# Optimization experiments

Hardware: AMD Instinct MI355X
Metric: run time of the kernel (lower is better)

Reference implementation:

```python
import jax, jax.numpy as jnp
import numpy as np
from jax import lax

UNITS = 64
LAYERS = 4

def _lstm_layer(x, Wx, U, b):
    # x: [B,T,F]; Keras gate order i,f,c,o; activation=relu, recurrent_activation=sigmoid
    B = x.shape[0]
    xz = jnp.einsum('btf,fg->btg', x, Wx) + b  # precompute input projections [B,T,4U]
    def step(carry, xz_t):
        h, c = carry
        z = xz_t + h @ U
        i, f, g, o = jnp.split(z, 4, axis=-1)
        c = jax.nn.sigmoid(f) * c + jax.nn.sigmoid(i) * jax.nn.relu(g)
        h = jax.nn.sigmoid(o) * jax.nn.relu(c)
        return (h, c), h
    h0 = jnp.zeros((B, UNITS), dtype=x.dtype)
    c0 = jnp.zeros((B, UNITS), dtype=x.dtype)
    _, hs = lax.scan(step, (h0, c0), jnp.swapaxes(xz, 0, 1))
    return jnp.swapaxes(hs, 0, 1)  # [B,T,U]

def setup_inputs() -> dict:
    key = jax.random.key(0)
    ks = jax.random.split(key, 1 + 3 * LAYERS + 2)
    B, T, F = 1024, 512, 1
    d = {'x': jax.random.normal(ks[0], (B, T, F), dtype=jnp.float32)}
    fin = F
    for l in range(LAYERS):
        d[f'Wx{l}'] = jax.random.normal(ks[1 + 3 * l], (fin, 4 * UNITS), dtype=jnp.float32) * 0.05
        d[f'U{l}'] = jax.random.normal(ks[2 + 3 * l], (UNITS, 4 * UNITS), dtype=jnp.float32) * 0.05
        d[f'b{l}'] = jnp.zeros((4 * UNITS,), dtype=jnp.float32)
        fin = UNITS
    d['Wd'] = jax.random.normal(ks[-2], (UNITS, 1), dtype=jnp.float32) * 0.05
    d['bd'] = jnp.zeros((1,), dtype=jnp.float32)
    return d

def reference(x, Wx0, U0, b0, Wx1, U1, b1, Wx2, U2, b2, Wx3, U3, b3, Wd, bd):
    # Dropout is identity at inference.
    h = x
    for Wx, U, b in ((Wx0, U0, b0), (Wx1, U1, b1), (Wx2, U2, b2), (Wx3, U3, b3)):
        h = _lstm_layer(h, Wx, U, b)
    h_last = h[:, -1, :]  # return_sequences=False on last LSTM
    return h_last @ Wd + bd  # [B,1]
```

## Files before the change

kernel.cpp:

```cpp
#include <hip/hip_runtime.h>
#include <stdint.h>

#define TT 512

typedef __fp16   f16x8  __attribute__((ext_vector_type(8)));
typedef float    f32x4  __attribute__((ext_vector_type(4)));
typedef __fp16   fp16x2 __attribute__((ext_vector_type(2)));
typedef uint32_t u32x2  __attribute__((ext_vector_type(2)));

__device__ __forceinline__ f32x4 mfma16(f16x8 a, f16x8 b, f32x4 c) {
    return __builtin_amdgcn_mfma_f32_16x16x32_f16(a, b, c, 0, 0, 0);
}
__device__ __forceinline__ uint32_t pkf16(float a, float b) {
    fp16x2 h = __builtin_amdgcn_cvt_pkrtz(a, b);
    return __builtin_bit_cast(uint32_t, h);
}

#define REP8(M) M(0)M(1)M(2)M(3)M(4)M(5)M(6)M(7)

#define GA(SRC, T, F) (f16x8){ \
  (__fp16)(SRC)[(32*(F)+8*quad+0)*256 + 16*(T)+l15], \
  (__fp16)(SRC)[(32*(F)+8*quad+1)*256 + 16*(T)+l15], \
  (__fp16)(SRC)[(32*(F)+8*quad+2)*256 + 16*(T)+l15], \
  (__fp16)(SRC)[(32*(F)+8*quad+3)*256 + 16*(T)+l15], \
  (__fp16)(SRC)[(32*(F)+8*quad+4)*256 + 16*(T)+l15], \
  (__fp16)(SRC)[(32*(F)+8*quad+5)*256 + 16*(T)+l15], \
  (__fp16)(SRC)[(32*(F)+8*quad+6)*256 + 16*(T)+l15], \
  (__fp16)(SRC)[(32*(F)+8*quad+7)*256 + 16*(T)+l15] }

#define DECLT(j) f16x8 uA##j##_0, uA##j##_1, wA##j##_0, wA##j##_1; f32x4 bias##j;
#define LOADT(j) { \
  const int Tg_ = ((j)>>1)*4 + 2*h + ((j)&1); \
  uA##j##_0 = GA(Uw, Tg_, 0); uA##j##_1 = GA(Uw, Tg_, 1); \
  bias##j = (f32x4){ bw_[16*Tg_ + 4*quad + 0], bw_[16*Tg_ + 4*quad + 1], \
                     bw_[16*Tg_ + 4*quad + 2], bw_[16*Tg_ + 4*quad + 3] }; \
  if (l > 0) { wA##j##_0 = GA(Wsrc, Tg_, 0); wA##j##_1 = GA(Wsrc, Tg_, 1); } \
  else { wA##j##_0 = __builtin_bit_cast(f16x8, (f32x4){ \
           Wx0[16*Tg_+4*quad+0], Wx0[16*Tg_+4*quad+1], \
           Wx0[16*Tg_+4*quad+2], Wx0[16*Tg_+4*quad+3] }); \
         wA##j##_1 = wA##j##_0; } }

#define MW0(j) acc##j = mfma16(wA##j##_0, xBp0, bias##j);
#define MW1(j) acc##j = mfma16(wA##j##_1, xBp1, acc##j);
#define MX(j)  acc##j = bias##j + __builtin_bit_cast(f32x4, wA##j##_0) * xvp4;
#define MU0(j) acc##j = mfma16(uA##j##_0, hB0, acc##j);
#define MU1(j) acc##j = mfma16(uA##j##_1, hB1, acc##j);

#define MFMA_SEG(t_) { \
  const __fp16* hp_ = hb_l + (((t_)-1)&3)*1152 + l15*72 + 8*quad; \
  f16x8 hB0 = *(const f16x8*)hp_; \
  f16x8 hB1 = *(const f16x8*)(hp_ + 32); \
  if (l > 0) { REP8(MW0) REP8(MW1) } \
  else       { f32x4 xvp4 = {xvp, xvp, xvp, xvp}; REP8(MX) } \
  REP8(MU0) \
  REP8(MU1) }

#define GATES(qp, Ai, Af, Ag, Ao, CST, SAVEK, HK) { \
  f32x4 ei_, ef_, eo_; \
  _Pragma("unroll") for (int r_ = 0; r_ < 4; ++r_) { \
    ei_[r_] = __builtin_amdgcn_exp2f(-1.4426950408889634f * Ai[r_]); \
    ef_[r_] = __builtin_amdgcn_exp2f(-1.4426950408889634f * Af[r_]); \
    eo_[r_] = __builtin_amdgcn_exp2f(-1.4426950408889634f * Ao[r_]); \
  } \
  f32x4 si_, sf_, so_; \
  _Pragma("unroll") for (int r_ = 0; r_ < 4; ++r_) { \
    si_[r_] = __builtin_amdgcn_rcpf(1.0f + ei_[r_]); \
    sf_[r_] = __builtin_amdgcn_rcpf(1.0f + ef_[r_]); \
    so_[r_] = __builtin_amdgcn_rcpf(1.0f + eo_[r_]); \
  } \
  const f32x4 z4_ = {0.f, 0.f, 0.f, 0.f}; \
  f32x4 rg_ = __builtin_elementwise_max(Ag, z4_); \
  f32x4 cv_ = sf_ * CST + si_ * rg_; \
  CST = cv_; \
  f32x4 hv_ = so_ * __builtin_elementwise_max(cv_, z4_); \
  u32x2 pv_ = { pkf16(hv_[0], hv_[1]), pkf16(hv_[2], hv_[3]) }; \
  *(u32x2*)(hw_ + 16*(qp)) = pv_; \
  if (SAVEK) HK = hv_; }

#define GATE_SEG(tg_, SV_) { \
  __fp16* hw_ = hb_l + ((tg_)&3)*1152 + l15*72 + 32*h + 4*quad; \
  GATES(0, acc0, acc2, acc4, acc6, cst0, SV_, hK0) \
  GATES(1, acc1, acc3, acc5, acc7, cst1, SV_, hK1) }

__global__ __launch_bounds__(512)
__attribute__((amdgpu_waves_per_eu(2, 2)))
void lstm_phase(
    const float* __restrict__ x,
    const float* __restrict__ Wx0, const float* __restrict__ U0, const float* __restrict__ b0,
    const float* __restrict__ Wx1, const float* __restrict__ U1, const float* __restrict__ b1,
    const float* __restrict__ Wx2, const float* __restrict__ U2, const float* __restrict__ b2,
    const float* __restrict__ Wx3, const float* __restrict__ U3, const float* __restrict__ b3,
    const float* __restrict__ Wd,  const float* __restrict__ bd,
    float* __restrict__ out)
{
    extern __shared__ uint32_t smem[];
    __fp16* hb16 = (__fp16*)smem;
    float*  xs   = (float*)(smem + 9216);
    float*  red  = (float*)(smem + 17920);

    const int tid  = threadIdx.x;
    const int lane = tid & 63;
    const int l15  = lane & 15;
    const int quad = lane >> 4;
    const int wv   = tid >> 6;
    const int l    = wv >> 1;
    const int h    = wv & 1;
    const int b0i  = blockIdx.x * 16;
    const bool phA = (l < 2);

    for (int i = tid; i < 9216; i += 512) smem[i] = 0;
    for (int i = tid; i < 16 * TT; i += 512) {
        int row = i >> 9, t_ = i & (TT - 1);
        xs[t_ * 17 + row] = x[(b0i + row) * TT + t_];
    }

    const float* Uw   = (l == 0) ? U0 : (l == 1) ? U1 : (l == 2) ? U2 : U3;
    const float* bw_  = (l == 0) ? b0 : (l == 1) ? b1 : (l == 2) ? b2 : b3;
    const float* Wsrc = (l == 1) ? Wx1 : (l == 2) ? Wx2 : (l == 3) ? Wx3 : U0;

    REP8(DECLT)
    REP8(LOADT)

    f32x4 acc0, acc1, acc2, acc3, acc4, acc5, acc6, acc7;
    f32x4 cst0 = {0,0,0,0}, cst1 = {0,0,0,0};
    f32x4 hK0  = {0,0,0,0}, hK1  = {0,0,0,0};

    __fp16* hb_l  = hb16 + l * 4608;
    const __fp16* hb_in = hb16 + (l > 0 ? (l - 1) * 4608 : 0);

    f16x8 xBp0 = {}, xBp1 = {};
    float xvp = 0.f;

    __syncthreads();

    if (l == 0) xvp = xs[l15];

    for (int s = 0; s < TT + 8; ++s) {
        if (phA) {
            const int t = s - 2 * l;
            if (t >= 0 && t < TT) MFMA_SEG(t)
        } else {
            const int tm = s - 2 * l;
            if (tm >= 0 && tm < TT) {
                const __fp16* xp_ = hb_in + (tm & 3) * 1152 + l15 * 72 + 8 * quad;
                xBp0 = *(const f16x8*)xp_;
                xBp1 = *(const f16x8*)(xp_ + 32);
            }
            const int tg = s - 1 - 2 * l;
            if (tg >= 0 && tg < TT) {
                const bool sv_ = (l == 3) && (tg == TT - 1);
                GATE_SEG(tg, sv_)
            }
        }
        __syncthreads();
        if (phA) {
            const int tn = s + 1 - 2 * l;
            if (tn >= 0 && tn < TT) {
                if (l > 0) {
                    const __fp16* xp_ = hb_in + (tn & 3) * 1152 + l15 * 72 + 8 * quad;
                    xBp0 = *(const f16x8*)xp_;
                    xBp1 = *(const f16x8*)(xp_ + 32);
                } else {
                    xvp = xs[tn * 17 + l15];
                }
            }
            const int t = s - 2 * l;
            if (t >= 0 && t < TT) GATE_SEG(t, false)
        } else {
            const int t = s - 2 * l;
            if (t >= 0 && t < TT) MFMA_SEG(t)
        }
        __syncthreads();
    }

    if (l == 3) {
        float p = 0.f;
        #pragma unroll
        for (int r = 0; r < 4; ++r) {
            p += hK0[r] * Wd[32 * h + 4 * quad + r];
            p += hK1[r] * Wd[32 * h + 16 + 4 * quad + r];
        }
        p += __shfl_down(p, 32, 64);
        p += __shfl_down(p, 16, 64);
        if (lane < 16) red[h * 16 + lane] = p;
    }
    __syncthreads();
    if (wv == 6 && lane < 16) out[b0i + lane] = red[lane] + red[16 + lane] + bd[0];
}

extern "C" void kernel_launch(void* const* d_in, const int* in_sizes, int n_in,
                              void* d_out, int out_size, void* d_ws, size_t ws_size,
                              hipStream_t stream) {
    const float* x   = (const float*)d_in[0];
    const float* Wx0 = (const float*)d_in[1];
    const float* U0  = (const float*)d_in[2];
    const float* b0  = (const float*)d_in[3];
    const float* Wx1 = (const float*)d_in[4];
    const float* U1  = (const float*)d_in[5];
    const float* b1  = (const float*)d_in[6];
    const float* Wx2 = (const float*)d_in[7];
    const float* U2  = (const float*)d_in[8];
    const float* b2  = (const float*)d_in[9];
    const float* Wx3 = (const float*)d_in[10];
    const float* U3  = (const float*)d_in[11];
    const float* b3  = (const float*)d_in[12];
    const float* Wd  = (const float*)d_in[13];
    const float* bd  = (const float*)d_in[14];
    float* out = (float*)d_out;

    static const int kLds = 17952 * 4;
    (void)hipFuncSetAttribute((const void*)lstm_phase,
                              hipFuncAttributeMaxDynamicSharedMemorySize, kLds);
    hipLaunchKernelGGL(lstm_phase, dim3(64), dim3(512), kLds, stream,
                       x, Wx0, U0, b0, Wx1, U1, b1, Wx2, U2, b2, Wx3, U3, b3,
                       Wd, bd, out);
}
```

Measured before the change: 691.9 us.

## Split each LSTM layer across four waves and move biases to LDS

Doubles the block to 1024 threads so each layer is handled by four waves instead of two. Each wave now owns one 16-column tile per gate rather than two, which halves the per-wave MFMA chain and gate math on the serial recurrence. Biases move from registers into shared memory and are reloaded every step, which frees registers for the higher waves-per-EU target. In exchange, more waves contend at every __syncthreads, and the final reduction now sums four partials.

```diff
diff --git a/kernel.cpp b/kernel.cpp
--- a/kernel.cpp
+++ b/kernel.cpp
@@ -16,7 +16,7 @@
     return __builtin_bit_cast(uint32_t, h);
 }
 
-#define REP8(M) M(0)M(1)M(2)M(3)M(4)M(5)M(6)M(7)
+#define REP4(M) M(0)M(1)M(2)M(3)
 
 #define GA(SRC, T, F) (f16x8){ \
   (__fp16)(SRC)[(32*(F)+8*quad+0)*256 + 16*(T)+l15], \
@@ -28,12 +28,10 @@
   (__fp16)(SRC)[(32*(F)+8*quad+6)*256 + 16*(T)+l15], \
   (__fp16)(SRC)[(32*(F)+8*quad+7)*256 + 16*(T)+l15] }
 
-#define DECLT(j) f16x8 uA##j##_0, uA##j##_1, wA##j##_0, wA##j##_1; f32x4 bias##j;
+#define DECLT(j) f16x8 uA##j##_0, uA##j##_1, wA##j##_0, wA##j##_1;
 #define LOADT(j) { \
-  const int Tg_ = ((j)>>1)*4 + 2*h + ((j)&1); \
+  const int Tg_ = 4*(j) + h2; \
   uA##j##_0 = GA(Uw, Tg_, 0); uA##j##_1 = GA(Uw, Tg_, 1); \
-  bias##j = (f32x4){ bw_[16*Tg_ + 4*quad + 0], bw_[16*Tg_ + 4*quad + 1], \
-                     bw_[16*Tg_ + 4*quad + 2], bw_[16*Tg_ + 4*quad + 3] }; \
   if (l > 0) { wA##j##_0 = GA(Wsrc, Tg_, 0); wA##j##_1 = GA(Wsrc, Tg_, 1); } \
   else { wA##j##_0 = __builtin_bit_cast(f16x8, (f32x4){ \
            Wx0[16*Tg_+4*quad+0], Wx0[16*Tg_+4*quad+1], \
@@ -47,15 +45,20 @@
 #define MU1(j) acc##j = mfma16(uA##j##_1, hB1, acc##j);
 
 #define MFMA_SEG(t_) { \
+  const float* bp_ = bs + l*256 + 16*h2 + 4*quad; \
+  f32x4 bias0 = *(const f32x4*)(bp_ +   0); \
+  f32x4 bias1 = *(const f32x4*)(bp_ +  64); \
+  f32x4 bias2 = *(const f32x4*)(bp_ + 128); \
+  f32x4 bias3 = *(const f32x4*)(bp_ + 192); \
   const __fp16* hp_ = hb_l + (((t_)-1)&3)*1152 + l15*72 + 8*quad; \
   f16x8 hB0 = *(const f16x8*)hp_; \
   f16x8 hB1 = *(const f16x8*)(hp_ + 32); \
-  if (l > 0) { REP8(MW0) REP8(MW1) } \
-  else       { f32x4 xvp4 = {xvp, xvp, xvp, xvp}; REP8(MX) } \
-  REP8(MU0) \
-  REP8(MU1) }
-
-#define GATES(qp, Ai, Af, Ag, Ao, CST, SAVEK, HK) { \
+  if (l > 0) { REP4(MW0) REP4(MW1) } \
+  else       { f32x4 xvp4 = {xvp, xvp, xvp, xvp}; REP4(MX) } \
+  REP4(MU0) \
+  REP4(MU1) }
+
+#define GATES(Ai, Af, Ag, Ao, CST, SAVEK, HK) { \
   f32x4 ei_, ef_, eo_; \
   _Pragma("unroll") for (int r_ = 0; r_ < 4; ++r_) { \
     ei_[r_] = __builtin_amdgcn_exp2f(-1.4426950408889634f * Ai[r_]); \
@@ -74,16 +77,15 @@
   CST = cv_; \
   f32x4 hv_ = so_ * __builtin_elementwise_max(cv_, z4_); \
   u32x2 pv_ = { pkf16(hv_[0], hv_[1]), pkf16(hv_[2], hv_[3]) }; \
-  *(u32x2*)(hw_ + 16*(qp)) = pv_; \
+  *(u32x2*)(hw_) = pv_; \
   if (SAVEK) HK = hv_; }
 
 #define GATE_SEG(tg_, SV_) { \
-  __fp16* hw_ = hb_l + ((tg_)&3)*1152 + l15*72 + 32*h + 4*quad; \
-  GATES(0, acc0, acc2, acc4, acc6, cst0, SV_, hK0) \
-  GATES(1, acc1, acc3, acc5, acc7, cst1, SV_, hK1) }
-
-__global__ __launch_bounds__(512)
-__attribute__((amdgpu_waves_per_eu(2, 2)))
+  __fp16* hw_ = hb_l + ((tg_)&3)*1152 + l15*72 + 16*h2 + 4*quad; \
+  GATES(acc0, acc1, acc2, acc3, cst0, SV_, hK0) }
+
+__global__ __launch_bounds__(1024)
+__attribute__((amdgpu_waves_per_eu(4, 4)))
 void lstm_phase(
     const float* __restrict__ x,
     const float* __restrict__ Wx0, const float* __restrict__ U0, const float* __restrict__ b0,
@@ -97,33 +99,38 @@
     __fp16* hb16 = (__fp16*)smem;
     float*  xs   = (float*)(smem + 9216);
     float*  red  = (float*)(smem + 17920);
+    float*  bs   = (float*)(smem + 17984);
 
     const int tid  = threadIdx.x;
     const int lane = tid & 63;
     const int l15  = lane & 15;
     const int quad = lane >> 4;
     const int wv   = tid >> 6;
-    const int l    = wv >> 1;
-    const int h    = wv & 1;
+    const int l    = wv >> 2;
+    const int h2   = wv & 3;
     const int b0i  = blockIdx.x * 16;
     const bool phA = (l < 2);
 
-    for (int i = tid; i < 9216; i += 512) smem[i] = 0;
-    for (int i = tid; i < 16 * TT; i += 512) {
+    for (int i = tid; i < 9216; i += 1024) smem[i] = 0;
+    for (int i = tid; i < 16 * TT; i += 1024) {
         int row = i >> 9, t_ = i & (TT - 1);
         xs[t_ * 17 + row] = x[(b0i + row) * TT + t_];
     }
+    {
+        int l_ = tid >> 8, c_ = tid & 255;
+        const float* bsrc = (l_ == 0) ? b0 : (l_ == 1) ? b1 : (l_ == 2) ? b2 : b3;
+        bs[tid] = bsrc[c_];
+    }
 
     const float* Uw   = (l == 0) ? U0 : (l == 1) ? U1 : (l == 2) ? U2 : U3;
-    const float* bw_  = (l == 0) ? b0 : (l == 1) ? b1 : (l == 2) ? b2 : b3;
     const float* Wsrc = (l == 1) ? Wx1 : (l == 2) ? Wx2 : (l == 3) ? Wx3 : U0;
 
-    REP8(DECLT)
-    REP8(LOADT)
-
-    f32x4 acc0, acc1, acc2, acc3, acc4, acc5, acc6, acc7;
-    f32x4 cst0 = {0,0,0,0}, cst1 = {0,0,0,0};
-    f32x4 hK0  = {0,0,0,0}, hK1  = {0,0,0,0};
+    REP4(DECLT)
+    REP4(LOADT)
+
+    f32x4 acc0, acc1, acc2, acc3;
+    f32x4 cst0 = {0,0,0,0};
+    f32x4 hK0  = {0,0,0,0};
 
     __fp16* hb_l  = hb16 + l * 4608;
     const __fp16* hb_in = hb16 + (l > 0 ? (l - 1) * 4608 : 0);
@@ -177,15 +184,15 @@
         float p = 0.f;
         #pragma unroll
         for (int r = 0; r < 4; ++r) {
-            p += hK0[r] * Wd[32 * h + 4 * quad + r];
-            p += hK1[r] * Wd[32 * h + 16 + 4 * quad + r];
+            p += hK0[r] * Wd[16 * h2 + 4 * quad + r];
         }
         p += __shfl_down(p, 32, 64);
         p += __shfl_down(p, 16, 64);
-        if (lane < 16) red[h * 16 + lane] = p;
+        if (lane < 16) red[h2 * 16 + lane] = p;
     }
     __syncthreads();
-    if (wv == 6 && lane < 16) out[b0i + lane] = red[lane] + red[16 + lane] + bd[0];
+    if (wv == 0 && lane < 16)
+        out[b0i + lane] = red[lane] + red[16 + lane] + red[32 + lane] + red[48 + lane] + bd[0];
 }
 
 extern "C" void kernel_launch(void* const* d_in, const int* in_sizes, int n_in,
@@ -208,10 +215,10 @@
     const float* bd  = (const float*)d_in[14];
     float* out = (float*)d_out;
 
-    static const int kLds = 17952 * 4;
+    static const int kLds = 19008 * 4;
     (void)hipFuncSetAttribute((const void*)lstm_phase,
                               hipFuncAttributeMaxDynamicSharedMemorySize, kLds);
-    hipLaunchKernelGGL(lstm_phase, dim3(64), dim3(512), kLds, stream,
+    hipLaunchKernelGGL(lstm_phase, dim3(64), dim3(1024), kLds, stream,
                        x, Wx0, U0, b0, Wx1, U1, b1, Wx2, U2, b2, Wx3, U3, b3,
                        Wd, bd, out);
 }
```

After: 741.9 us. +7.2%, slower.

## Replace block-wide barriers with per-wave LDS flag handshakes in LSTM wavefront

Applied to the files above, without the earlier changes.

Drops the two __syncthreads per step of the phased layer pipeline. Each wave now publishes a progress counter in LDS with release stores and waits on acquire loads of only its dependencies: the previous layer, its sibling half-wave, and the next layer's consumption. The hidden-state ring buffer grows from 4 to 8 slots so producers can run ahead, which lets layers drift relative to each other instead of moving in lockstep. The cost is spin-wait polling on LDS and a larger LDS footprint, plus the risk of subtle ordering bugs in the handshake.

```diff
diff --git a/kernel.cpp b/kernel.cpp
--- a/kernel.cpp
+++ b/kernel.cpp
@@ -47,7 +47,7 @@
 #define MU1(j) acc##j = mfma16(uA##j##_1, hB1, acc##j);
 
 #define MFMA_SEG(t_) { \
-  const __fp16* hp_ = hb_l + (((t_)-1)&3)*1152 + l15*72 + 8*quad; \
+  const __fp16* hp_ = hb_l + (((t_)-1)&7)*1152 + l15*72 + 8*quad; \
   f16x8 hB0 = *(const f16x8*)hp_; \
   f16x8 hB1 = *(const f16x8*)(hp_ + 32); \
   if (l > 0) { REP8(MW0) REP8(MW1) } \
@@ -78,9 +78,13 @@
   if (SAVEK) HK = hv_; }
 
 #define GATE_SEG(tg_, SV_) { \
-  __fp16* hw_ = hb_l + ((tg_)&3)*1152 + l15*72 + 32*h + 4*quad; \
+  __fp16* hw_ = hb_l + ((tg_)&7)*1152 + l15*72 + 32*h + 4*quad; \
   GATES(0, acc0, acc2, acc4, acc6, cst0, SV_, hK0) \
   GATES(1, acc1, acc3, acc5, acc7, cst1, SV_, hK1) }
+
+#define WAITGE(cache, idx, need) \
+  while ((cache) < (need)) \
+    (cache) = __hip_atomic_load(&Pf[idx], __ATOMIC_ACQUIRE, __HIP_MEMORY_SCOPE_WORKGROUP);
 
 __global__ __launch_bounds__(512)
 __attribute__((amdgpu_waves_per_eu(2, 2)))
@@ -95,8 +99,9 @@
 {
     extern __shared__ uint32_t smem[];
     __fp16* hb16 = (__fp16*)smem;
-    float*  xs   = (float*)(smem + 9216);
-    float*  red  = (float*)(smem + 17920);
+    float*  xs   = (float*)(smem + 18432);
+    float*  red  = (float*)(smem + 27136);
+    int*    Pf   = (int*)(smem + 27168);
 
     const int tid  = threadIdx.x;
     const int lane = tid & 63;
@@ -106,9 +111,9 @@
     const int l    = wv >> 1;
     const int h    = wv & 1;
     const int b0i  = blockIdx.x * 16;
-    const bool phA = (l < 2);
-
-    for (int i = tid; i < 9216; i += 512) smem[i] = 0;
+
+    for (int i = tid; i < 27176; i += 512) smem[i] = 0;
+    __syncthreads();
     for (int i = tid; i < 16 * TT; i += 512) {
         int row = i >> 9, t_ = i & (TT - 1);
         xs[t_ * 17 + row] = x[(b0i + row) * TT + t_];
@@ -125,8 +130,8 @@
     f32x4 cst0 = {0,0,0,0}, cst1 = {0,0,0,0};
     f32x4 hK0  = {0,0,0,0}, hK1  = {0,0,0,0};
 
-    __fp16* hb_l  = hb16 + l * 4608;
-    const __fp16* hb_in = hb16 + (l > 0 ? (l - 1) * 4608 : 0);
+    __fp16* hb_l  = hb16 + l * 9216;
+    const __fp16* hb_in = hb16 + (l > 0 ? (l - 1) * 9216 : 0);
 
     f16x8 xBp0 = {}, xBp1 = {};
     float xvp = 0.f;
@@ -135,43 +140,31 @@
 
     if (l == 0) xvp = xs[l15];
 
-    for (int s = 0; s < TT + 8; ++s) {
-        if (phA) {
-            const int t = s - 2 * l;
-            if (t >= 0 && t < TT) MFMA_SEG(t)
-        } else {
-            const int tm = s - 2 * l;
-            if (tm >= 0 && tm < TT) {
-                const __fp16* xp_ = hb_in + (tm & 3) * 1152 + l15 * 72 + 8 * quad;
-                xBp0 = *(const f16x8*)xp_;
-                xBp1 = *(const f16x8*)(xp_ + 32);
-            }
-            const int tg = s - 1 - 2 * l;
-            if (tg >= 0 && tg < TT) {
-                const bool sv_ = (l == 3) && (tg == TT - 1);
-                GATE_SEG(tg, sv_)
-            }
-        }
-        __syncthreads();
-        if (phA) {
-            const int tn = s + 1 - 2 * l;
-            if (tn >= 0 && tn < TT) {
-                if (l > 0) {
-                    const __fp16* xp_ = hb_in + (tn & 3) * 1152 + l15 * 72 + 8 * quad;
-                    xBp0 = *(const f16x8*)xp_;
-                    xBp1 = *(const f16x8*)(xp_ + 32);
-                } else {
-                    xvp = xs[tn * 17 + l15];
-                }
-            }
-            const int t = s - 2 * l;
-            if (t >= 0 && t < TT) GATE_SEG(t, false)
-        } else {
-            const int t = s - 2 * l;
-            if (t >= 0 && t < TT) MFMA_SEG(t)
-        }
-        __syncthreads();
+    int pA0 = 0, pA1 = 0, pP = 0, pC0 = 0, pC1 = 0;
+
+    for (int t = 0; t < TT; ++t) {
+        if (l > 0) {
+            WAITGE(pA0, 2*l - 2, t + 1)
+            WAITGE(pA1, 2*l - 1, t + 1)
+            const __fp16* xp_ = hb_in + (t & 7) * 1152 + l15 * 72 + 8 * quad;
+            xBp0 = *(const f16x8*)xp_;
+            xBp1 = *(const f16x8*)(xp_ + 32);
+        }
+        if (t > 0) WAITGE(pP, 2*l + 1 - h, t)
+        if (l < 3 && t >= 8) {
+            WAITGE(pC0, 2*l + 2, t - 7)
+            WAITGE(pC1, 2*l + 3, t - 7)
+        }
+        MFMA_SEG(t)
+        {
+            const bool sv_ = (l == 3) && (t == TT - 1);
+            GATE_SEG(t, sv_)
+        }
+        __hip_atomic_store(&Pf[2*l + h], t + 1, __ATOMIC_RELEASE, __HIP_MEMORY_SCOPE_WORKGROUP);
+        if (l == 0 && t + 1 < TT) xvp = xs[(t + 1) * 17 + l15];
     }
+
+    __syncthreads();
 
     if (l == 3) {
         float p = 0.f;
@@ -208,7 +201,7 @@
     const float* bd  = (const float*)d_in[14];
     float* out = (float*)d_out;
 
-    static const int kLds = 17952 * 4;
+    static const int kLds = 27176 * 4;
     (void)hipFuncSetAttribute((const void*)lstm_phase,
                               hipFuncAttributeMaxDynamicSharedMemorySize, kLds);
     hipLaunchKernelGGL(lstm_phase, dim3(64), dim3(512), kLds, stream,
```

Measured after the change: 648.8 us. 6.2% less time.
